# Kernel optimization log

Measured on AMD Instinct MI355X. Metric: run time of the kernel, lower is better.

Reference implementation:

```python
import jax, jax.numpy as jnp
import numpy as np

N = 32768          # n_atoms
E = 524288         # n_edges (avg degree 16)
MUL = 8            # multiplicity of 0e and 1o in irreps_in/out
NB = 8             # n_basis
HR = 64            # hidden_radial
NTP = 4 * MUL * MUL  # tensor-product weight_numel (4 CG paths)
AVG_NEI = 16.0
INV_SQRT3 = 1.0 / np.sqrt(3.0)      # w3j(1,1,0) component
ALPHA = 1.0 / np.sqrt(2.0 * MUL)    # path normalization: fan_in = 2 paths * mul_in*mul_sh


def setup_inputs() -> dict:
    key = jax.random.key(0)
    ks = jax.random.split(key, 12)
    h = jax.random.normal(ks[0], (N, 4 * MUL), jnp.float32)            # [N, 8 scalars + 8*3 vectors]
    edge_index = jax.random.randint(ks[1], (2, E), 0, N)               # [2, E] int
    edge_sh = jax.random.normal(ks[2], (E, 4), jnp.float32)            # [E, 1x0e + 1x1o]
    edge_radial = jax.random.uniform(ks[3], (E, NB), jnp.float32)      # [E, n_basis]

    def lin(k, fi, fo):
        return (jax.random.normal(k, (fi, fo), jnp.float32) / np.sqrt(fi)).astype(jnp.float32)

    W1 = lin(ks[4], NB, HR); b1 = jnp.zeros((HR,), jnp.float32)
    W2 = lin(ks[5], HR, HR); b2 = jnp.zeros((HR,), jnp.float32)
    W3 = lin(ks[6], HR, NTP); b3 = jnp.zeros((NTP,), jnp.float32)
    Ws = jax.random.normal(ks[7], (MUL, MUL), jnp.float32)             # self-interaction, scalar block
    Wv = jax.random.normal(ks[8], (MUL, MUL), jnp.float32)             # self-interaction, vector block
    return dict(h=h, edge_index=edge_index, edge_sh=edge_sh, edge_radial=edge_radial,
                n_atoms=N, W1=W1, b1=b1, W2=W2, b2=b2, W3=W3, b3=b3, Ws=Ws, Wv=Wv)


def reference(h, edge_index, edge_sh, edge_radial, n_atoms, W1, b1, W2, b2, W3, b3, Ws, Wv):
    src, dst = edge_index[0], edge_index[1]

    # radial MLP -> per-edge tensor-product weights [E, 256]
    x = jax.nn.silu(edge_radial @ W1 + b1)
    x = jax.nn.silu(x @ W2 + b2)
    tpw = x @ W3 + b3
    P = MUL * MUL
    W00  = tpw[:, 0 * P:1 * P].reshape(-1, MUL, MUL)  # 0e x 0e -> 0e
    W110 = tpw[:, 1 * P:2 * P].reshape(-1, MUL, MUL)  # 1o x 1o -> 0e (dot)
    W01  = tpw[:, 2 * P:3 * P].reshape(-1, MUL, MUL)  # 0e x 1o -> 1o
    W10  = tpw[:, 3 * P:4 * P].reshape(-1, MUL, MUL)  # 1o x 0e -> 1o

    hs = h[:, :MUL]                         # [N, 8] scalars
    hv = h[:, MUL:].reshape(-1, MUL, 3)     # [N, 8, 3] vectors
    hs_e = hs[src]                          # gather [E, 8]
    hv_e = hv[src]                          # gather [E, 8, 3]
    sh0 = edge_sh[:, 0]                     # [E]
    sh1 = edge_sh[:, 1:4]                   # [E, 3]

    # equivariant tensor product (e3nn FullyConnectedTensorProduct, l<=1)
    m0 = ALPHA * (jnp.einsum('eu,euw->ew', hs_e * sh0[:, None], W00)
                  + INV_SQRT3 * jnp.einsum('eui,ei,euw->ew', hv_e, sh1, W110))       # [E, 8]
    m1 = ALPHA * (jnp.einsum('eu,ei,euw->ewi', hs_e, sh1, W01)
                  + jnp.einsum('eui,euw->ewi', hv_e * sh0[:, None, None], W10))      # [E, 8, 3]
    messages = jnp.concatenate([m0, m1.reshape(-1, 3 * MUL)], axis=-1)               # [E, 32]

    # scatter-add to destination nodes, degree normalization
    agg = jax.ops.segment_sum(messages, dst, num_segments=n_atoms) / np.sqrt(AVG_NEI)

    # self interaction (o3.Linear: block-diagonal per irrep, 1/sqrt(fan_in))
    self0 = (hs @ Ws) / np.sqrt(MUL)
    self1 = jnp.einsum('nui,uw->nwi', hv, Wv) / np.sqrt(MUL)
    h_self = jnp.concatenate([self0, self1.reshape(-1, 3 * MUL)], axis=-1)

    return h_self + agg
```

## Files before the change

kernel.cpp:

```cpp
#include <hip/hip_runtime.h>

#define N_ATOMS 32768
#define E_EDGES 524288
#define FEAT 32
#define TPB 512
#define WPB 8
#define PASSES 8
#define GRID (E_EDGES / (WPB * PASSES * 16))
#define INV_SQRT3 0.57735026919f
#define MSG_SCALE 0.0625f
#define SELF_SCALE 0.35355339059f

#define WS_MSG   0
#define WS_CNT   33554432
#define WS_CUR   33685504
#define WS_OFFS  33816576
#define WS_BSUM  33947648
#define WS_BBASE 33948160
#define WS_EIDS  33948672
#define WS_WF    36045824

typedef _Float16 f16;
typedef __attribute__((ext_vector_type(8))) _Float16 f16x8;
typedef __attribute__((ext_vector_type(4))) float f32x4;
typedef __attribute__((ext_vector_type(2))) _Float16 f16x2;
typedef __attribute__((ext_vector_type(4))) _Float16 f16x4;

__device__ __forceinline__ float silu(float x) { return x / (1.0f + __expf(-x)); }

__device__ __forceinline__ f32x4 mfma16(f16x8 a, f16x8 b, f32x4 c) {
    return __builtin_amdgcn_mfma_f32_16x16x32_f16(a, b, c, 0, 0, 0);
}

__global__ __launch_bounds__(256) void prep_kernel(
    const float* __restrict__ W1, const float* __restrict__ W2,
    const float* __restrict__ W3, f16* __restrict__ wf)
{
    int idx = blockIdx.x * 256 + threadIdx.x;
    float v;
    if (idx < 2048) {
        int f = idx;
        int n0 = f >> 9, lane = (f >> 3) & 63, j = f & 7;
        int k = ((lane >> 4) << 3) + j, n = (n0 << 4) + (lane & 15);
        v = (k < 8) ? W1[k * 64 + n] : 0.0f;
    } else if (idx < 6144) {
        int f = idx - 2048;
        int kk = f >> 11, n0 = (f >> 9) & 3, lane = (f >> 3) & 63, j = f & 7;
        int k = (kk << 5) + ((lane >> 4) << 3) + j, n = (n0 << 4) + (lane & 15);
        v = W2[k * 64 + n];
    } else {
        int f = idx - 6144;
        int kk = f >> 13, n0 = (f >> 9) & 15, lane = (f >> 3) & 63, j = f & 7;
        int k = (kk << 5) + ((lane >> 4) << 3) + j, n = (n0 << 4) + (lane & 15);
        v = W3[k * 256 + n];
    }
    wf[idx] = (f16)v;
}

__global__ __launch_bounds__(256) void count_kernel(const int* __restrict__ eidx,
                                                    int* __restrict__ cnt) {
    int e = blockIdx.x * 256 + threadIdx.x;
    atomicAdd(&cnt[eidx[E_EDGES + e]], 1);
}

__global__ __launch_bounds__(256) void scan1_kernel(const int* __restrict__ cnt,
                                                    int* __restrict__ bsum) {
    __shared__ int s[256];
    int t = threadIdx.x;
    s[t] = cnt[blockIdx.x * 256 + t];
    __syncthreads();
    for (int d = 128; d > 0; d >>= 1) {
        if (t < d) s[t] += s[t + d];
        __syncthreads();
    }
    if (t == 0) bsum[blockIdx.x] = s[0];
}

__global__ __launch_bounds__(64) void scan2_kernel(const int* __restrict__ bsum,
                                                   int* __restrict__ bbase) {
    int lane = threadIdx.x;
    int v0 = bsum[2 * lane], v1 = bsum[2 * lane + 1];
    int s = v0 + v1, x = s;
    for (int d = 1; d < 64; d <<= 1) {
        int y = __shfl_up(x, d, 64);
        if (lane >= d) x += y;
    }
    int excl = x - s;
    bbase[2 * lane] = excl;
    bbase[2 * lane + 1] = excl + v0;
}

__global__ __launch_bounds__(256) void scan3_kernel(const int* __restrict__ cnt,
                                                    const int* __restrict__ bbase,
                                                    int* __restrict__ offs) {
    int t = threadIdx.x, lane = t & 63, w = t >> 6;
    int v = cnt[blockIdx.x * 256 + t];
    int x = v;
    for (int d = 1; d < 64; d <<= 1) {
        int y = __shfl_up(x, d, 64);
        if (lane >= d) x += y;
    }
    __shared__ int wsum[4];
    if (lane == 63) wsum[w] = x;
    __syncthreads();
    int base = bbase[blockIdx.x];
    for (int i = 0; i < w; ++i) base += wsum[i];
    offs[blockIdx.x * 256 + t] = base + x - v;
}

__global__ __launch_bounds__(256) void fill_kernel(const int* __restrict__ eidx,
                                                   const int* __restrict__ offs,
                                                   int* __restrict__ cur,
                                                   int* __restrict__ eids) {
    int e = blockIdx.x * 256 + threadIdx.x;
    int d = eidx[E_EDGES + e];
    int slot = atomicAdd(&cur[d], 1);
    eids[offs[d] + slot] = e;
}

__global__ __launch_bounds__(TPB, 4) void edge_kernel(
    const float* __restrict__ h, const int* __restrict__ eidx,
    const float* __restrict__ esh, const float* __restrict__ erad,
    const f16* __restrict__ wf, const int* __restrict__ eids,
    const float* __restrict__ b1, const float* __restrict__ b2,
    const float* __restrict__ b3,
    f16* __restrict__ msg)
{
    __shared__ f16x8 wL[2816];
    __shared__ float b1s[64], b2s[64], b3s[256];
    __shared__ __align__(16) char xtp[WPB][16 * 72 * 2];

    const int tid = threadIdx.x;
    {
        const f16x8* wfv = (const f16x8*)wf;
#pragma unroll
        for (int i = 0; i < 5; ++i)
            wL[tid + i * TPB] = wfv[tid + i * TPB];
        int i5 = tid + 5 * TPB;
        if (i5 < 2816) wL[i5] = wfv[i5];
        if (tid < 64) { b1s[tid] = b1[tid]; b2s[tid] = b2[tid]; }
        if (tid < 256) b3s[tid] = b3[tid];
    }
    __syncthreads();

    const f16x8* w1f = wL;
    const f16x8* w2f = wL + 256;
    const f16x8* w3f = wL + 768;

    const int wave = tid >> 6, lane = tid & 63;
    const int g = lane >> 4, m = lane & 15;
    const int me = lane >> 2, w0 = (lane & 3) * 2;

    f16* xs = (f16*)&xtp[wave][0];
    float* tpt = (float*)&xtp[wave][0];

    for (int pass = 0; pass < PASSES; ++pass) {
        const int tile = (blockIdx.x * WPB + wave) * PASSES + pass;
        const int j0 = tile * 16;

        const int eidM = eids[j0 + m];
        const int eidE = eids[j0 + me];

        const int src = eidx[eidE];
        const float4 shv = *(const float4*)(esh + (long)eidE * 4);
        float hrow[32];
        {
            const float* hp = h + (long)src * FEAT;
#pragma unroll
            for (int c4 = 0; c4 < 8; ++c4)
                ((float4*)hrow)[c4] = ((const float4*)hp)[c4];
        }

        f16x8 arad;
        {
            float r[8] = {0.f, 0.f, 0.f, 0.f, 0.f, 0.f, 0.f, 0.f};
            if (g == 0) {
                const float4* rp = (const float4*)(erad + (long)eidM * 8);
                float4 r0 = rp[0], r1 = rp[1];
                r[0] = r0.x; r[1] = r0.y; r[2] = r0.z; r[3] = r0.w;
                r[4] = r1.x; r[5] = r1.y; r[6] = r1.z; r[7] = r1.w;
            }
#pragma unroll
            for (int j = 0; j < 8; ++j) arad[j] = (f16)r[j];
        }

#pragma unroll
        for (int n0 = 0; n0 < 4; ++n0) {
            f32x4 acc = {};
            acc = mfma16(arad, w1f[n0 * 64 + lane], acc);
            float bn = b1s[n0 * 16 + m];
#pragma unroll
            for (int q = 0; q < 4; ++q) {
                float v = silu(acc[q] + bn);
                xs[(g * 4 + q) * 72 + n0 * 16 + m] = (f16)v;
            }
        }
        f16x8 a2[2];
        a2[0] = *(const f16x8*)(xs + m * 72 + g * 8);
        a2[1] = *(const f16x8*)(xs + m * 72 + 32 + g * 8);

#pragma unroll
        for (int n0 = 0; n0 < 4; ++n0) {
            f32x4 acc = {};
            acc = mfma16(a2[0], w2f[n0 * 64 + lane], acc);
            acc = mfma16(a2[1], w2f[(4 + n0) * 64 + lane], acc);
            float bn = b2s[n0 * 16 + m];
#pragma unroll
            for (int q = 0; q < 4; ++q) {
                float v = silu(acc[q] + bn);
                xs[(g * 4 + q) * 72 + n0 * 16 + m] = (f16)v;
            }
        }
        f16x8 a3[2];
        a3[0] = *(const f16x8*)(xs + m * 72 + g * 8);
        a3[1] = *(const f16x8*)(xs + m * 72 + 32 + g * 8);

        float m0a0 = 0.f, m0a1 = 0.f, s20 = 0.f, s21 = 0.f;
        float sv[6] = {0.f, 0.f, 0.f, 0.f, 0.f, 0.f};

#pragma unroll
        for (int t = 0; t < 16; ++t) {
            const int c = t >> 2, n0 = t & 3;
            f32x4 acc = {};
            acc = mfma16(a3[0], w3f[(c * 4 + n0) * 64 + lane], acc);
            acc = mfma16(a3[1], w3f[(16 + c * 4 + n0) * 64 + lane], acc);
            float bn = b3s[c * 64 + n0 * 16 + m];
            float* tb = tpt + (t & 1) * 288;
#pragma unroll
            for (int q = 0; q < 4; ++q)
                tb[(g * 4 + q) * 18 + m] = acc[q] + bn;
            if (t > 0) {
                const int tp = t - 1, cp = tp >> 2, np = tp & 3;
                const float* rb = tpt + (tp & 1) * 288;
#pragma unroll
                for (int uu = 0; uu < 2; ++uu) {
                    const int u = 2 * np + uu;
                    float2 tv = *(const float2*)(rb + me * 18 + uu * 8 + w0);
                    if (cp == 0) {
                        float a0 = hrow[u] * shv.x;
                        m0a0 += a0 * tv.x; m0a1 += a0 * tv.y;
                    } else if (cp == 1) {
                        float a1 = INV_SQRT3 * (hrow[8 + u * 3] * shv.y +
                                                hrow[9 + u * 3] * shv.z +
                                                hrow[10 + u * 3] * shv.w);
                        m0a0 += a1 * tv.x; m0a1 += a1 * tv.y;
                    } else if (cp == 2) {
                        s20 += hrow[u] * tv.x; s21 += hrow[u] * tv.y;
                    } else {
                        sv[0] += hrow[8 + u * 3] * tv.x;
                        sv[1] += hrow[9 + u * 3] * tv.x;
                        sv[2] += hrow[10 + u * 3] * tv.x;
                        sv[3] += hrow[8 + u * 3] * tv.y;
                        sv[4] += hrow[9 + u * 3] * tv.y;
                        sv[5] += hrow[10 + u * 3] * tv.y;
                    }
                }
            }
        }
        {
            const float* rb = tpt + 288;
#pragma unroll
            for (int uu = 0; uu < 2; ++uu) {
                const int u = 6 + uu;
                float2 tv = *(const float2*)(rb + me * 18 + uu * 8 + w0);
                sv[0] += hrow[8 + u * 3] * tv.x;
                sv[1] += hrow[9 + u * 3] * tv.x;
                sv[2] += hrow[10 + u * 3] * tv.x;
                sv[3] += hrow[8 + u * 3] * tv.y;
                sv[4] += hrow[9 + u * 3] * tv.y;
                sv[5] += hrow[10 + u * 3] * tv.y;
            }
        }

        f16* row = msg + (long)(j0 + me) * FEAT;
        f16x2 p0;
        p0[0] = (f16)(MSG_SCALE * m0a0);
        p0[1] = (f16)(MSG_SCALE * m0a1);
        *(f16x2*)(row + w0) = p0;
        f16 m1v[6];
#pragma unroll
        for (int i = 0; i < 3; ++i) {
            float s1i = (i == 0) ? shv.y : (i == 1) ? shv.z : shv.w;
            m1v[i]     = (f16)(MSG_SCALE * (s1i * s20 + shv.x * sv[i]));
            m1v[3 + i] = (f16)(MSG_SCALE * (s1i * s21 + shv.x * sv[3 + i]));
        }
        f16* rp = row + 8 + 3 * w0;
        { f16x2 t2; t2[0] = m1v[0]; t2[1] = m1v[1]; *(f16x2*)(rp)     = t2; }
        { f16x2 t2; t2[0] = m1v[2]; t2[1] = m1v[3]; *(f16x2*)(rp + 2) = t2; }
        { f16x2 t2; t2[0] = m1v[4]; t2[1] = m1v[5]; *(f16x2*)(rp + 4) = t2; }
    }
}

__global__ __launch_bounds__(256) void gather_kernel(
    const f16* __restrict__ msg,
    const int* __restrict__ offs, const int* __restrict__ cnt,
    const float* __restrict__ h,
    const float* __restrict__ Ws, const float* __restrict__ Wv,
    float* __restrict__ out)
{
    const int t = threadIdx.x;
    const int n = blockIdx.x * 32 + (t >> 3);
    const int L = t & 7;
    const int base = offs[n], deg = cnt[n];

    float a0 = 0.f, a1 = 0.f, a2 = 0.f, a3 = 0.f;
    float c0 = 0.f, c1 = 0.f, c2 = 0.f, c3 = 0.f;
    int i = 0;
    for (; i + 1 < deg; i += 2) {
        f16x4 v = *(const f16x4*)(msg + (long)(base + i) * FEAT + L * 4);
        f16x4 w = *(const f16x4*)(msg + (long)(base + i + 1) * FEAT + L * 4);
        a0 += (float)v[0]; a1 += (float)v[1]; a2 += (float)v[2]; a3 += (float)v[3];
        c0 += (float)w[0]; c1 += (float)w[1]; c2 += (float)w[2]; c3 += (float)w[3];
    }
    if (i < deg) {
        f16x4 v = *(const f16x4*)(msg + (long)(base + i) * FEAT + L * 4);
        a0 += (float)v[0]; a1 += (float)v[1]; a2 += (float)v[2]; a3 += (float)v[3];
    }
    a0 += c0; a1 += c1; a2 += c2; a3 += c3;

    const float* hrow = h + (long)n * FEAT;
    const int f0 = L * 4;
    float o[4];
    if (L < 2) {
#pragma unroll
        for (int j = 0; j < 4; ++j) {
            int w = f0 + j;
            float a = 0.f;
#pragma unroll
            for (int u = 0; u < 8; ++u) a += hrow[u] * Ws[u * 8 + w];
            o[j] = SELF_SCALE * a;
        }
    } else {
#pragma unroll
        for (int j = 0; j < 4; ++j) {
            int f = f0 + j, w = (f - 8) / 3, i3 = (f - 8) % 3;
            float a = 0.f;
#pragma unroll
            for (int u = 0; u < 8; ++u) a += hrow[8 + u * 3 + i3] * Wv[u * 8 + w];
            o[j] = SELF_SCALE * a;
        }
    }
    float4 r;
    r.x = o[0] + a0; r.y = o[1] + a1; r.z = o[2] + a2; r.w = o[3] + a3;
    *(float4*)(out + (long)n * FEAT + f0) = r;
}

extern "C" void kernel_launch(void* const* d_in, const int* in_sizes, int n_in,
                              void* d_out, int out_size, void* d_ws, size_t ws_size,
                              hipStream_t stream)
{
    const float* h    = (const float*)d_in[0];
    const int*   eidx = (const int*)  d_in[1];
    const float* esh  = (const float*)d_in[2];
    const float* erad = (const float*)d_in[3];
    const float* W1   = (const float*)d_in[5];
    const float* b1   = (const float*)d_in[6];
    const float* W2   = (const float*)d_in[7];
    const float* b2   = (const float*)d_in[8];
    const float* W3   = (const float*)d_in[9];
    const float* b3   = (const float*)d_in[10];
    const float* Ws   = (const float*)d_in[11];
    const float* Wv   = (const float*)d_in[12];
    float* out = (float*)d_out;

    char* ws = (char*)d_ws;
    f16* msg   = (f16*)(ws + WS_MSG);
    int* cnt   = (int*)(ws + WS_CNT);
    int* cur   = (int*)(ws + WS_CUR);
    int* offs  = (int*)(ws + WS_OFFS);
    int* bsum  = (int*)(ws + WS_BSUM);
    int* bbase = (int*)(ws + WS_BBASE);
    int* eids  = (int*)(ws + WS_EIDS);
    f16* wf    = (f16*)(ws + WS_WF);

    hipMemsetAsync(cnt, 0, 2 * N_ATOMS * sizeof(int), stream);

    prep_kernel<<<88, 256, 0, stream>>>(W1, W2, W3, wf);
    count_kernel<<<E_EDGES / 256, 256, 0, stream>>>(eidx, cnt);
    scan1_kernel<<<N_ATOMS / 256, 256, 0, stream>>>(cnt, bsum);
    scan2_kernel<<<1, 64, 0, stream>>>(bsum, bbase);
    scan3_kernel<<<N_ATOMS / 256, 256, 0, stream>>>(cnt, bbase, offs);
    fill_kernel<<<E_EDGES / 256, 256, 0, stream>>>(eidx, offs, cur, eids);
    edge_kernel<<<GRID, TPB, 0, stream>>>(h, eidx, esh, erad, wf, eids,
                                          b1, b2, b3, msg);
    gather_kernel<<<N_ATOMS / 32, 256, 0, stream>>>(msg, offs, cnt,
                                                    h, Ws, Wv, out);
}
```

Measured before the change: 158.3 us.

## Merge prep and count kernels, single-block scan, transpose TP staging layout

Folds the weight-repack kernel and the degree-count kernel into one launch, and replaces the three-kernel prefix scan with one 1024-thread block that scans 32 counts per thread. This removes several small launches and their inter-kernel gaps. Separately, the per-warp staging of tensor-product weights is changed to a stride-20 transposed layout with one vector store per lane and scalar reads, aimed at fewer LDS bank conflicts. The single-block scan serializes 32K elements on one CU, and the new LDS read pattern may trade conflicts on writes for conflicts on reads.

```diff
diff --git a/kernel.cpp b/kernel.cpp
--- a/kernel.cpp
+++ b/kernel.cpp
@@ -15,10 +15,11 @@
 #define WS_CNT   33554432
 #define WS_CUR   33685504
 #define WS_OFFS  33816576
-#define WS_BSUM  33947648
-#define WS_BBASE 33948160
 #define WS_EIDS  33948672
 #define WS_WF    36045824
+
+#define TSTR 20
+#define TBUF 320
 
 typedef _Float16 f16;
 typedef __attribute__((ext_vector_type(8))) _Float16 f16x8;
@@ -32,80 +33,71 @@
     return __builtin_amdgcn_mfma_f32_16x16x32_f16(a, b, c, 0, 0, 0);
 }
 
-__global__ __launch_bounds__(256) void prep_kernel(
+__global__ __launch_bounds__(256) void prepcount_kernel(
     const float* __restrict__ W1, const float* __restrict__ W2,
-    const float* __restrict__ W3, f16* __restrict__ wf)
-{
-    int idx = blockIdx.x * 256 + threadIdx.x;
-    float v;
-    if (idx < 2048) {
-        int f = idx;
-        int n0 = f >> 9, lane = (f >> 3) & 63, j = f & 7;
-        int k = ((lane >> 4) << 3) + j, n = (n0 << 4) + (lane & 15);
-        v = (k < 8) ? W1[k * 64 + n] : 0.0f;
-    } else if (idx < 6144) {
-        int f = idx - 2048;
-        int kk = f >> 11, n0 = (f >> 9) & 3, lane = (f >> 3) & 63, j = f & 7;
-        int k = (kk << 5) + ((lane >> 4) << 3) + j, n = (n0 << 4) + (lane & 15);
-        v = W2[k * 64 + n];
+    const float* __restrict__ W3, f16* __restrict__ wf,
+    const int* __restrict__ eidx, int* __restrict__ cnt)
+{
+    const int b = blockIdx.x;
+    if (b < 88) {
+        int idx = b * 256 + threadIdx.x;
+        if (idx >= 22528) return;
+        float v;
+        if (idx < 2048) {
+            int f = idx;
+            int n0 = f >> 9, lane = (f >> 3) & 63, j = f & 7;
+            int k = ((lane >> 4) << 3) + j, n = (n0 << 4) + (lane & 15);
+            v = (k < 8) ? W1[k * 64 + n] : 0.0f;
+        } else if (idx < 6144) {
+            int f = idx - 2048;
+            int kk = f >> 11, n0 = (f >> 9) & 3, lane = (f >> 3) & 63, j = f & 7;
+            int k = (kk << 5) + ((lane >> 4) << 3) + j, n = (n0 << 4) + (lane & 15);
+            v = W2[k * 64 + n];
+        } else {
+            int f = idx - 6144;
+            int kk = f >> 13, n0 = (f >> 9) & 15, lane = (f >> 3) & 63, j = f & 7;
+            int k = (kk << 5) + ((lane >> 4) << 3) + j, n = (n0 << 4) + (lane & 15);
+            v = W3[k * 256 + n];
+        }
+        wf[idx] = (f16)v;
     } else {
-        int f = idx - 6144;
-        int kk = f >> 13, n0 = (f >> 9) & 15, lane = (f >> 3) & 63, j = f & 7;
-        int k = (kk << 5) + ((lane >> 4) << 3) + j, n = (n0 << 4) + (lane & 15);
-        v = W3[k * 256 + n];
-    }
-    wf[idx] = (f16)v;
-}
-
-__global__ __launch_bounds__(256) void count_kernel(const int* __restrict__ eidx,
-                                                    int* __restrict__ cnt) {
-    int e = blockIdx.x * 256 + threadIdx.x;
-    atomicAdd(&cnt[eidx[E_EDGES + e]], 1);
-}
-
-__global__ __launch_bounds__(256) void scan1_kernel(const int* __restrict__ cnt,
-                                                    int* __restrict__ bsum) {
-    __shared__ int s[256];
-    int t = threadIdx.x;
-    s[t] = cnt[blockIdx.x * 256 + t];
-    __syncthreads();
-    for (int d = 128; d > 0; d >>= 1) {
-        if (t < d) s[t] += s[t + d];
-        __syncthreads();
-    }
-    if (t == 0) bsum[blockIdx.x] = s[0];
-}
-
-__global__ __launch_bounds__(64) void scan2_kernel(const int* __restrict__ bsum,
-                                                   int* __restrict__ bbase) {
-    int lane = threadIdx.x;
-    int v0 = bsum[2 * lane], v1 = bsum[2 * lane + 1];
-    int s = v0 + v1, x = s;
+        int e = (b - 88) * 256 + threadIdx.x;
+        atomicAdd(&cnt[eidx[E_EDGES + e]], 1);
+    }
+}
+
+__global__ __launch_bounds__(1024) void scan_kernel(const int* __restrict__ cnt,
+                                                    int* __restrict__ offs)
+{
+    const int t = threadIdx.x, lane = t & 63, w = t >> 6;
+    int4 v[8];
+    int s = 0;
+#pragma unroll
+    for (int j = 0; j < 8; ++j) {
+        v[j] = *(const int4*)(cnt + t * 32 + j * 4);
+        s += v[j].x + v[j].y + v[j].z + v[j].w;
+    }
+    int x = s;
+#pragma unroll
     for (int d = 1; d < 64; d <<= 1) {
         int y = __shfl_up(x, d, 64);
         if (lane >= d) x += y;
     }
-    int excl = x - s;
-    bbase[2 * lane] = excl;
-    bbase[2 * lane + 1] = excl + v0;
-}
-
-__global__ __launch_bounds__(256) void scan3_kernel(const int* __restrict__ cnt,
-                                                    const int* __restrict__ bbase,
-                                                    int* __restrict__ offs) {
-    int t = threadIdx.x, lane = t & 63, w = t >> 6;
-    int v = cnt[blockIdx.x * 256 + t];
-    int x = v;
-    for (int d = 1; d < 64; d <<= 1) {
-        int y = __shfl_up(x, d, 64);
-        if (lane >= d) x += y;
-    }
-    __shared__ int wsum[4];
+    __shared__ int wsum[16];
     if (lane == 63) wsum[w] = x;
     __syncthreads();
-    int base = bbase[blockIdx.x];
+    int base = 0;
     for (int i = 0; i < w; ++i) base += wsum[i];
-    offs[blockIdx.x * 256 + t] = base + x - v;
+    int run = base + x - s;
+#pragma unroll
+    for (int j = 0; j < 8; ++j) {
+        int4 o;
+        o.x = run; run += v[j].x;
+        o.y = run; run += v[j].y;
+        o.z = run; run += v[j].z;
+        o.w = run; run += v[j].w;
+        *(int4*)(offs + t * 32 + j * 4) = o;
+    }
 }
 
 __global__ __launch_bounds__(256) void fill_kernel(const int* __restrict__ eidx,
@@ -128,7 +120,7 @@
 {
     __shared__ f16x8 wL[2816];
     __shared__ float b1s[64], b2s[64], b3s[256];
-    __shared__ __align__(16) char xtp[WPB][16 * 72 * 2];
+    __shared__ __align__(16) char xtp[WPB][2560];
 
     const int tid = threadIdx.x;
     {
@@ -225,50 +217,52 @@
             acc = mfma16(a3[0], w3f[(c * 4 + n0) * 64 + lane], acc);
             acc = mfma16(a3[1], w3f[(16 + c * 4 + n0) * 64 + lane], acc);
             float bn = b3s[c * 64 + n0 * 16 + m];
-            float* tb = tpt + (t & 1) * 288;
-#pragma unroll
-            for (int q = 0; q < 4; ++q)
-                tb[(g * 4 + q) * 18 + m] = acc[q] + bn;
+            f32x4 av;
+#pragma unroll
+            for (int q = 0; q < 4; ++q) av[q] = acc[q] + bn;
+            *(f32x4*)(tpt + (t & 1) * TBUF + m * TSTR + g * 4) = av;
             if (t > 0) {
                 const int tp = t - 1, cp = tp >> 2, np = tp & 3;
-                const float* rb = tpt + (tp & 1) * 288;
+                const float* rb = tpt + (tp & 1) * TBUF;
 #pragma unroll
                 for (int uu = 0; uu < 2; ++uu) {
                     const int u = 2 * np + uu;
-                    float2 tv = *(const float2*)(rb + me * 18 + uu * 8 + w0);
+                    float tx = rb[(uu * 8 + w0) * TSTR + me];
+                    float ty = rb[(uu * 8 + w0 + 1) * TSTR + me];
                     if (cp == 0) {
                         float a0 = hrow[u] * shv.x;
-                        m0a0 += a0 * tv.x; m0a1 += a0 * tv.y;
+                        m0a0 += a0 * tx; m0a1 += a0 * ty;
                     } else if (cp == 1) {
                         float a1 = INV_SQRT3 * (hrow[8 + u * 3] * shv.y +
                                                 hrow[9 + u * 3] * shv.z +
                                                 hrow[10 + u * 3] * shv.w);
-                        m0a0 += a1 * tv.x; m0a1 += a1 * tv.y;
+                        m0a0 += a1 * tx; m0a1 += a1 * ty;
                     } else if (cp == 2) {
-                        s20 += hrow[u] * tv.x; s21 += hrow[u] * tv.y;
+                        s20 += hrow[u] * tx; s21 += hrow[u] * ty;
                     } else {
-                        sv[0] += hrow[8 + u * 3] * tv.x;
-                        sv[1] += hrow[9 + u * 3] * tv.x;
-                        sv[2] += hrow[10 + u * 3] * tv.x;
-                        sv[3] += hrow[8 + u * 3] * tv.y;
-                        sv[4] += hrow[9 + u * 3] * tv.y;
-                        sv[5] += hrow[10 + u * 3] * tv.y;
+                        sv[0] += hrow[8 + u * 3] * tx;
+                        sv[1] += hrow[9 + u * 3] * tx;
+                        sv[2] += hrow[10 + u * 3] * tx;
+                        sv[3] += hrow[8 + u * 3] * ty;
+                        sv[4] += hrow[9 + u * 3] * ty;
+                        sv[5] += hrow[10 + u * 3] * ty;
                     }
                 }
             }
         }
         {
-            const float* rb = tpt + 288;
+            const float* rb = tpt + TBUF;
 #pragma unroll
             for (int uu = 0; uu < 2; ++uu) {
                 const int u = 6 + uu;
-                float2 tv = *(const float2*)(rb + me * 18 + uu * 8 + w0);
-                sv[0] += hrow[8 + u * 3] * tv.x;
-                sv[1] += hrow[9 + u * 3] * tv.x;
-                sv[2] += hrow[10 + u * 3] * tv.x;
-                sv[3] += hrow[8 + u * 3] * tv.y;
-                sv[4] += hrow[9 + u * 3] * tv.y;
-                sv[5] += hrow[10 + u * 3] * tv.y;
+                float tx = rb[(uu * 8 + w0) * TSTR + me];
+                float ty = rb[(uu * 8 + w0 + 1) * TSTR + me];
+                sv[0] += hrow[8 + u * 3] * tx;
+                sv[1] += hrow[9 + u * 3] * tx;
+                sv[2] += hrow[10 + u * 3] * tx;
+                sv[3] += hrow[8 + u * 3] * ty;
+                sv[4] += hrow[9 + u * 3] * ty;
+                sv[5] += hrow[10 + u * 3] * ty;
             }
         }
 
@@ -368,18 +362,14 @@
     int* cnt   = (int*)(ws + WS_CNT);
     int* cur   = (int*)(ws + WS_CUR);
     int* offs  = (int*)(ws + WS_OFFS);
-    int* bsum  = (int*)(ws + WS_BSUM);
-    int* bbase = (int*)(ws + WS_BBASE);
     int* eids  = (int*)(ws + WS_EIDS);
     f16* wf    = (f16*)(ws + WS_WF);
 
     hipMemsetAsync(cnt, 0, 2 * N_ATOMS * sizeof(int), stream);
 
-    prep_kernel<<<88, 256, 0, stream>>>(W1, W2, W3, wf);
-    count_kernel<<<E_EDGES / 256, 256, 0, stream>>>(eidx, cnt);
-    scan1_kernel<<<N_ATOMS / 256, 256, 0, stream>>>(cnt, bsum);
-    scan2_kernel<<<1, 64, 0, stream>>>(bsum, bbase);
-    scan3_kernel<<<N_ATOMS / 256, 256, 0, stream>>>(cnt, bbase, offs);
+    prepcount_kernel<<<88 + E_EDGES / 256, 256, 0, stream>>>(W1, W2, W3, wf,
+                                                             eidx, cnt);
+    scan_kernel<<<1, 1024, 0, stream>>>(cnt, offs);
     fill_kernel<<<E_EDGES / 256, 256, 0, stream>>>(eidx, offs, cur, eids);
     edge_kernel<<<GRID, TPB, 0, stream>>>(h, eidx, esh, erad, wf, eids,
                                           b1, b2, b3, msg);
```

Measured after the change: 565.1 us. 3.57x slower.
